# Kernel tuning notes

Measured on AMD Instinct MI355X. Metric: run time of the kernel, lower is better.

The kernel has to match this reference:

```python
import jax, jax.numpy as jnp
import numpy as np

WIN = 11      # window_size in pytorch_msssim
SIGMA = 1.5   # gaussian sigma in create_window
LEVELS = 5


def _gauss_window(channels, dtype):
    # 1D gaussian -> normalized 2D window, replicated per channel for depthwise conv
    x = jnp.arange(WIN, dtype=dtype) - WIN // 2
    g = jnp.exp(-(x * x) / (2.0 * SIGMA * SIGMA))
    g = g / jnp.sum(g)
    w2 = jnp.outer(g, g)  # [11,11]
    return jnp.broadcast_to(w2[None, None], (channels, 1, WIN, WIN))


def _dwconv(x, w):
    # depthwise valid conv, NCHW (matches F.conv2d(..., padding=0, groups=channel))
    return jax.lax.conv_general_dilated(
        x, w, window_strides=(1, 1), padding='VALID',
        dimension_numbers=('NCHW', 'OIHW', 'NCHW'),
        feature_group_count=x.shape[1])


def _ssim_cs(p, t, w):
    # pytorch_msssim.ssim with full=True, val_range L=1 (inputs in [0,1])
    C1 = 0.01 ** 2
    C2 = 0.03 ** 2
    mu1 = _dwconv(p, w)
    mu2 = _dwconv(t, w)
    mu1_sq = mu1 * mu1
    mu2_sq = mu2 * mu2
    mu1_mu2 = mu1 * mu2
    sigma1_sq = _dwconv(p * p, w) - mu1_sq
    sigma2_sq = _dwconv(t * t, w) - mu2_sq
    sigma12 = _dwconv(p * t, w) - mu1_mu2
    v1 = 2.0 * sigma12 + C2
    v2 = sigma1_sq + sigma2_sq + C2
    # per-category means (axis 1 = the 10 categories, batched as channels)
    cs = jnp.mean(v1 / v2, axis=(0, 2, 3))                                   # [C]
    sim = jnp.mean(((2.0 * mu1_mu2 + C1) * v1) / ((mu1_sq + mu2_sq + C1) * v2),
                   axis=(0, 2, 3))                                           # [C]
    return sim, cs


def _avg_pool2(x):
    n, c, h, w = x.shape
    return x.reshape(n, c, h // 2, 2, w // 2, 2).mean(axis=(3, 5))


def setup_inputs() -> dict:
    key = jax.random.key(0)
    k1, k2 = jax.random.split(key)
    y_pred = jax.random.uniform(k1, (10, 1024, 1024), dtype=jnp.float32)
    y_true = jax.random.uniform(k2, (10, 1024, 1024), dtype=jnp.float32)
    return {"y_pred": y_pred, "y_true": y_true}


def reference(y_pred, y_true):
    # MSSLoss.forward: loss = sum over 10 categories of msssim(pred[c], true[c]);
    # return 1 - mean(loss)  (loss is a scalar, so mean is identity).
    # All 10 per-category msssim calls are batched as channels of one depthwise conv.
    dtype = y_pred.dtype
    weights = jnp.array([0.0448, 0.2856, 0.3001, 0.2363, 0.1333], dtype=dtype)
    p = y_pred[None]  # [1,10,H,W]
    t = y_true[None]
    w = _gauss_window(p.shape[1], dtype)
    sims, css = [], []
    for _ in range(LEVELS):
        s, c = _ssim_cs(p, t, w)
        sims.append(s)
        css.append(c)
        p = _avg_pool2(p)
        t = _avg_pool2(t)
    mssim = jnp.stack(sims)  # [5, 10]
    mcs = jnp.stack(css)     # [5, 10]
    pow1 = mcs ** weights[:, None]
    pow2 = mssim ** weights[:, None]
    # Po-Hsun-Su pytorch_msssim: output = torch.prod(pow1[:-1] * pow2[-1])
    per_cat = jnp.prod(pow1[:-1] * pow2[-1][None, :], axis=0)  # [10]
    return 1.0 - jnp.sum(per_cat)
```

## Files before the change

### kernel.cpp

```cpp
#include <hip/hip_runtime.h>
#include <cstddef>

#define WIN 11
#define HALO 10
#define NCH 10

typedef float v4f __attribute__((ext_vector_type(4)));

constexpr float Gc[WIN] = {
    0.00102838f, 0.00759876f, 0.03600077f, 0.10936069f, 0.21300554f,
    0.26601173f, 0.21300554f, 0.10936069f, 0.03600077f, 0.00759876f,
    0.00102838f};

constexpr int HPITCH = 33;
constexpr int RS = 76;
constexpr int RSZ = RS * HPITCH;

struct Ptrs {
    const float* p[5];
    const float* t[5];
};

__global__ __launch_bounds__(256) void pool_all(
    const float* __restrict__ P0, const float* __restrict__ T0,
    float* __restrict__ p1, float* __restrict__ t1,
    float* __restrict__ p2, float* __restrict__ t2,
    float* __restrict__ p3, float* __restrict__ t3,
    float* __restrict__ p4, float* __restrict__ t4,
    float* __restrict__ acc) {
    __shared__ float sp2[256], st2[256], sp3[64], st3[64];
    const int tid = threadIdx.x;
    if (blockIdx.x == 0 && tid < 128) acc[tid] = 0.f;

    const int b = blockIdx.x;
    const int bx = b & 15, by = (b >> 4) & 15, ch = b >> 8;
    const int tx = tid & 15, ty = tid >> 4;

    const size_t rbase =
        ((size_t)ch * 1024 + by * 64 + ty * 4) * 1024 + bx * 64 + tx * 4;
    float4 pr[4], tr[4];
#pragma unroll
    for (int r2 = 0; r2 < 4; ++r2) {
        pr[r2] = *(const float4*)(P0 + rbase + (size_t)r2 * 1024);
        tr[r2] = *(const float4*)(T0 + rbase + (size_t)r2 * 1024);
    }
    float p1a = 0.25f * ((pr[0].x + pr[0].y) + (pr[1].x + pr[1].y));
    float p1b = 0.25f * ((pr[0].z + pr[0].w) + (pr[1].z + pr[1].w));
    float p1c = 0.25f * ((pr[2].x + pr[2].y) + (pr[3].x + pr[3].y));
    float p1d = 0.25f * ((pr[2].z + pr[2].w) + (pr[3].z + pr[3].w));
    float t1a = 0.25f * ((tr[0].x + tr[0].y) + (tr[1].x + tr[1].y));
    float t1b = 0.25f * ((tr[0].z + tr[0].w) + (tr[1].z + tr[1].w));
    float t1c = 0.25f * ((tr[2].x + tr[2].y) + (tr[3].x + tr[3].y));
    float t1d = 0.25f * ((tr[2].z + tr[2].w) + (tr[3].z + tr[3].w));
    size_t o1 = ((size_t)ch * 512 + by * 32 + ty * 2) * 512 + bx * 32 + tx * 2;
    *(float2*)(p1 + o1) = make_float2(p1a, p1b);
    *(float2*)(p1 + o1 + 512) = make_float2(p1c, p1d);
    *(float2*)(t1 + o1) = make_float2(t1a, t1b);
    *(float2*)(t1 + o1 + 512) = make_float2(t1c, t1d);
    float p2v = 0.25f * ((p1a + p1b) + (p1c + p1d));
    float t2v = 0.25f * ((t1a + t1b) + (t1c + t1d));
    size_t o2 = ((size_t)ch * 256 + by * 16 + ty) * 256 + bx * 16 + tx;
    p2[o2] = p2v;
    t2[o2] = t2v;
    sp2[tid] = p2v;
    st2[tid] = t2v;
    __syncthreads();
    if (tid < 64) {
        int x3 = tid & 7, y3 = tid >> 3;
        int i0 = (2 * y3) * 16 + 2 * x3;
        float p3v = 0.25f * ((sp2[i0] + sp2[i0 + 1]) + (sp2[i0 + 16] + sp2[i0 + 17]));
        float t3v = 0.25f * ((st2[i0] + st2[i0 + 1]) + (st2[i0 + 16] + st2[i0 + 17]));
        size_t o3 = ((size_t)ch * 128 + by * 8 + y3) * 128 + bx * 8 + x3;
        p3[o3] = p3v;
        t3[o3] = t3v;
        sp3[tid] = p3v;
        st3[tid] = t3v;
    }
    __syncthreads();
    if (tid < 16) {
        int x4 = tid & 3, y4 = tid >> 2;
        int i0 = (2 * y4) * 8 + 2 * x4;
        float p4v = 0.25f * ((sp3[i0] + sp3[i0 + 1]) + (sp3[i0 + 8] + sp3[i0 + 9]));
        float t4v = 0.25f * ((st3[i0] + st3[i0 + 1]) + (st3[i0 + 8] + st3[i0 + 9]));
        size_t o4 = ((size_t)ch * 64 + by * 4 + y4) * 64 + bx * 4 + x4;
        p4[o4] = p4v;
        t4[o4] = t4v;
    }
}

__global__ __launch_bounds__(256) void ssim_strip(Ptrs ptrs,
                                                  float* __restrict__ acc) {
    __shared__ v4f hq[RSZ];
    __shared__ float red[8];

    const int bxi = blockIdx.x;
    int lvl, base;
    if (bxi < 128)      { lvl = 0; base = 0; }
    else if (bxi < 160) { lvl = 1; base = 128; }
    else if (bxi < 168) { lvl = 2; base = 160; }
    else if (bxi < 172) { lvl = 3; base = 168; }
    else                { lvl = 4; base = 172; }
    const int local = bxi - base;
    const int H = 1024 >> lvl;
    const int Wout = H - HALO;
    const int ncol = 32 >> lvl;
    const int cs = local & (ncol - 1);
    const int rsi = local >> (5 - lvl);
    const int X0 = cs * 32;
    const int strip_y0 = rsi * 256;
    const int strip_rows = min(256, Wout - strip_y0);
    const int rows_needed = strip_rows + HALO;
    const int nIter = (strip_rows + 31) >> 5;

    const int c = blockIdx.y;
    const float* Pc = ptrs.p[lvl] + (size_t)c * H * H;
    const float* Tc = ptrs.t[lvl] + (size_t)c * H * H;
    const int tid = threadIdx.x;

    auto load_row18 = [&](int gy, int gxb, float2 lp[9], float2 lt[9]) {
        const float* Pr = Pc + (size_t)gy * H + gxb;
        const float* Tr = Tc + (size_t)gy * H + gxb;
        if (gxb + 18 <= H) {
#pragma unroll
            for (int j = 0; j < 9; ++j) {
                lp[j] = *(const float2*)(Pr + 2 * j);
                lt[j] = *(const float2*)(Tr + 2 * j);
            }
        } else {
#pragma unroll
            for (int j = 0; j < 9; ++j) {
                float2 a = make_float2(0.f, 0.f), b = make_float2(0.f, 0.f);
                if (gxb + 2 * j < H)     { a.x = Pr[2 * j];     b.x = Tr[2 * j]; }
                if (gxb + 2 * j + 1 < H) { a.y = Pr[2 * j + 1]; b.y = Tr[2 * j + 1]; }
                lp[j] = a;
                lt[j] = b;
            }
        }
    };

    auto conv_store8 = [&](int rr, int x0, const float2 lp[9], const float2 lt[9]) {
        v4f aq[8] = {};
#pragma unroll
        for (int xi = 0; xi < 18; ++xi) {
            float pv = (xi & 1) ? lp[xi >> 1].y : lp[xi >> 1].x;
            float tv = (xi & 1) ? lt[xi >> 1].y : lt[xi >> 1].x;
            v4f xq = (v4f){pv, tv, pv * pv + tv * tv, pv * tv};
#pragma unroll
            for (int o = 0; o < 8; ++o) {
                int k = xi - o;
                if (k >= 0 && k <= 10) aq[o] = aq[o] + Gc[k] * xq;
            }
        }
        const int sb = rr * HPITCH + x0;
#pragma unroll
        for (int o = 0; o < 8; ++o) hq[sb + o] = aq[o];
    };

    {
        const int r = tid >> 2, seg = tid & 3;
        if (r < 42) {
            float2 lp[9], lt[9];
            load_row18(strip_y0 + r, X0 + 8 * seg, lp, lt);
            conv_store8(r, 8 * seg, lp, lt);
        }
    }

    const bool isProd = (tid >= 128);
    const int pr = tid & 31;
    const int pseg = (tid >> 5) & 3;
    float2 plp[9], plt[9];
    int prRow = 42 + pr;
    int prSlot = prRow;
    bool pHave = false;
    if (isProd && prRow < rows_needed && nIter > 1) {
        load_row18(strip_y0 + prRow, X0 + 8 * pseg, plp, plt);
        pHave = true;
    }
    __syncthreads();

    float cs_sum = 0.f, sim_sum = 0.f;
    const int txl = tid & 31;
    const int g = (tid >> 5) & 3;
    int y0m = 0;
    for (int i = 0; i < nIter; ++i) {
        if (isProd) {
            if (pHave) conv_store8(prSlot, 8 * pseg, plp, plt);
            prSlot += 32;
            if (prSlot >= RS) prSlot -= RS;
            prRow += 32;
            pHave = (prRow < rows_needed) && (i + 2 < nIter + 1) && (i + 1 < nIter);
            if (pHave) load_row18(strip_y0 + prRow, X0 + 8 * pseg, plp, plt);
        } else {
            int sl = y0m + 8 * g;
            if (sl >= RS) sl -= RS;
            v4f a[8] = {};
#pragma unroll
            for (int yr = 0; yr < 18; ++yr) {
                v4f vq = hq[sl * HPITCH + txl];
#pragma unroll
                for (int o = 0; o < 8; ++o) {
                    int k = yr - o;
                    if (k >= 0 && k <= 10) a[o] = a[o] + Gc[k] * vq;
                }
                ++sl;
                if (sl >= RS) sl = 0;
            }
            const float C1c = 1.0e-4f, C2c = 9.0e-4f;
            const bool colok = (X0 + txl) < Wout;
            const int orow0 = 32 * i + 8 * g;
#pragma unroll
            for (int o = 0; o < 8; ++o) {
                if (colok && (orow0 + o) < strip_rows) {
                    float mu1 = a[o].x, mu2 = a[o].y;
                    float mu1s = mu1 * mu1, mu2s = mu2 * mu2, mu12 = mu1 * mu2;
                    float v2 = a[o].z - mu1s - mu2s + C2c;
                    float v1 = 2.f * (a[o].w - mu12) + C2c;
                    float den2 = mu1s + mu2s + C1c;
                    float num2 = 2.f * mu12 + C1c;
                    float inv = 1.f / (v2 * den2);
                    cs_sum = fmaf(v1 * den2, inv, cs_sum);
                    sim_sum = fmaf(num2 * v1, inv, sim_sum);
                }
            }
        }
        y0m += 32;
        if (y0m >= RS) y0m -= RS;
        __syncthreads();
    }

#pragma unroll
    for (int off = 32; off > 0; off >>= 1) {
        cs_sum += __shfl_down(cs_sum, off, 64);
        sim_sum += __shfl_down(sim_sum, off, 64);
    }
    int wave = tid >> 6;
    if ((tid & 63) == 0) {
        red[wave * 2 + 0] = sim_sum;
        red[wave * 2 + 1] = cs_sum;
    }
    __syncthreads();
    if (tid == 0) {
        float s = red[0] + red[2] + red[4] + red[6];
        float cc = red[1] + red[3] + red[5] + red[7];
        atomicAdd(&acc[(lvl * NCH + c) * 2 + 0], s);
        atomicAdd(&acc[(lvl * NCH + c) * 2 + 1], cc);
    }
}

__global__ void finalize_k(const float* __restrict__ acc, float* __restrict__ out) {
    if (threadIdx.x != 0) return;
    const double w[5] = {0.0448, 0.2856, 0.3001, 0.2363, 0.1333};
    const double counts[5] = {1014.0 * 1014.0, 502.0 * 502.0, 246.0 * 246.0,
                              118.0 * 118.0, 54.0 * 54.0};
    double total = 0.0;
    for (int c = 0; c < NCH; ++c) {
        double pc = 1.0;
        for (int l = 0; l < 4; ++l) {
            double mcs = (double)acc[(l * NCH + c) * 2 + 1] / counts[l];
            pc *= pow(mcs, w[l]);
        }
        double ms4 = (double)acc[(4 * NCH + c) * 2 + 0] / counts[4];
        double p2 = pow(ms4, w[4]);
        pc *= (p2 * p2) * (p2 * p2);
        total += pc;
    }
    *out = (float)(1.0 - total);
}

extern "C" void kernel_launch(void* const* d_in, const int* in_sizes, int n_in,
                              void* d_out, int out_size, void* d_ws, size_t ws_size,
                              hipStream_t stream) {
    const float* P0 = (const float*)d_in[0];
    const float* T0 = (const float*)d_in[1];
    float* out = (float*)d_out;
    float* acc = (float*)d_ws;

    const size_t n1 = (size_t)NCH * 512 * 512;
    const size_t n2 = (size_t)NCH * 256 * 256;
    const size_t n3 = (size_t)NCH * 128 * 128;
    const size_t n4 = (size_t)NCH * 64 * 64;
    float* p1 = acc + 128;
    float* t1 = p1 + n1;
    float* p2 = t1 + n1;
    float* t2 = p2 + n2;
    float* p3 = t2 + n2;
    float* t3 = p3 + n3;
    float* p4 = t3 + n3;
    float* t4 = p4 + n4;

    pool_all<<<2560, 256, 0, stream>>>(P0, T0, p1, t1, p2, t2, p3, t3, p4, t4, acc);

    Ptrs ptrs;
    ptrs.p[0] = P0; ptrs.t[0] = T0;
    ptrs.p[1] = p1; ptrs.t[1] = t1;
    ptrs.p[2] = p2; ptrs.t[2] = t2;
    ptrs.p[3] = p3; ptrs.t[3] = t3;
    ptrs.p[4] = p4; ptrs.t[4] = t4;

    ssim_strip<<<dim3(174, NCH, 1), 256, 0, stream>>>(ptrs, acc);

    finalize_k<<<1, 64, 0, stream>>>(acc, out);
}
```

Before: 198.0 us.

## Shrink per-thread output tile to 4 and ring buffer to 42 rows for occupancy

Cuts each thread's horizontal and vertical convolution work from 8 outputs to 4. The shared-memory ring buffer shrinks from 76 to 42 rows and each pipeline iteration now covers 16 rows instead of 32. A launch-bounds occupancy hint of 7 blocks per CU is added, and rows are loaded with float4 vector loads. Smaller register arrays and less LDS per block allow more resident waves, at the cost of more halo recomputation per output (14 inputs for 4 outputs versus 18 for 8) and twice as many barrier-synchronized iterations.

Measured after the change: 389.6 us. 1.97x slower.

```diff
diff --git a/kernel.cpp b/kernel.cpp
--- a/kernel.cpp
+++ b/kernel.cpp
@@ -13,7 +13,7 @@
     0.00102838f};
 
 constexpr int HPITCH = 33;
-constexpr int RS = 76;
+constexpr int RS = 42;
 constexpr int RSZ = RS * HPITCH;
 
 struct Ptrs {
@@ -88,8 +88,8 @@
     }
 }
 
-__global__ __launch_bounds__(256) void ssim_strip(Ptrs ptrs,
-                                                  float* __restrict__ acc) {
+__global__ __launch_bounds__(256, 7) void ssim_strip(Ptrs ptrs,
+                                                     float* __restrict__ acc) {
     __shared__ v4f hq[RSZ];
     __shared__ float red[8];
 
@@ -110,70 +110,82 @@
     const int strip_y0 = rsi * 256;
     const int strip_rows = min(256, Wout - strip_y0);
     const int rows_needed = strip_rows + HALO;
-    const int nIter = (strip_rows + 31) >> 5;
+    const int nIter = (strip_rows + 15) >> 4;
 
     const int c = blockIdx.y;
     const float* Pc = ptrs.p[lvl] + (size_t)c * H * H;
     const float* Tc = ptrs.t[lvl] + (size_t)c * H * H;
     const int tid = threadIdx.x;
 
-    auto load_row18 = [&](int gy, int gxb, float2 lp[9], float2 lt[9]) {
+    auto load_row14 = [&](int gy, int gxb, float lp[14], float lt[14]) {
         const float* Pr = Pc + (size_t)gy * H + gxb;
         const float* Tr = Tc + (size_t)gy * H + gxb;
-        if (gxb + 18 <= H) {
-#pragma unroll
-            for (int j = 0; j < 9; ++j) {
-                lp[j] = *(const float2*)(Pr + 2 * j);
-                lt[j] = *(const float2*)(Tr + 2 * j);
+        if (gxb + 14 <= H) {
+            float4 a0 = *(const float4*)(Pr);
+            float4 a1 = *(const float4*)(Pr + 4);
+            float4 a2 = *(const float4*)(Pr + 8);
+            float2 a3 = *(const float2*)(Pr + 12);
+            lp[0] = a0.x; lp[1] = a0.y; lp[2]  = a0.z; lp[3]  = a0.w;
+            lp[4] = a1.x; lp[5] = a1.y; lp[6]  = a1.z; lp[7]  = a1.w;
+            lp[8] = a2.x; lp[9] = a2.y; lp[10] = a2.z; lp[11] = a2.w;
+            lp[12] = a3.x; lp[13] = a3.y;
+            float4 b0 = *(const float4*)(Tr);
+            float4 b1 = *(const float4*)(Tr + 4);
+            float4 b2 = *(const float4*)(Tr + 8);
+            float2 b3 = *(const float2*)(Tr + 12);
+            lt[0] = b0.x; lt[1] = b0.y; lt[2]  = b0.z; lt[3]  = b0.w;
+            lt[4] = b1.x; lt[5] = b1.y; lt[6]  = b1.z; lt[7]  = b1.w;
+            lt[8] = b2.x; lt[9] = b2.y; lt[10] = b2.z; lt[11] = b2.y;
+            lt[11] = b2.w;
+            lt[12] = b3.x; lt[13] = b3.y;
+        } else {
+#pragma unroll
+            for (int j = 0; j < 14; ++j) {
+                float pv = 0.f, tv = 0.f;
+                if (gxb + j < H) { pv = Pr[j]; tv = Tr[j]; }
+                lp[j] = pv;
+                lt[j] = tv;
             }
-        } else {
-#pragma unroll
-            for (int j = 0; j < 9; ++j) {
-                float2 a = make_float2(0.f, 0.f), b = make_float2(0.f, 0.f);
-                if (gxb + 2 * j < H)     { a.x = Pr[2 * j];     b.x = Tr[2 * j]; }
-                if (gxb + 2 * j + 1 < H) { a.y = Pr[2 * j + 1]; b.y = Tr[2 * j + 1]; }
-                lp[j] = a;
-                lt[j] = b;
-            }
         }
     };
 
-    auto conv_store8 = [&](int rr, int x0, const float2 lp[9], const float2 lt[9]) {
-        v4f aq[8] = {};
-#pragma unroll
-        for (int xi = 0; xi < 18; ++xi) {
-            float pv = (xi & 1) ? lp[xi >> 1].y : lp[xi >> 1].x;
-            float tv = (xi & 1) ? lt[xi >> 1].y : lt[xi >> 1].x;
+    auto conv_store4 = [&](int rr, int x0, const float lp[14], const float lt[14]) {
+        v4f aq[4] = {};
+#pragma unroll
+        for (int xi = 0; xi < 14; ++xi) {
+            float pv = lp[xi];
+            float tv = lt[xi];
             v4f xq = (v4f){pv, tv, pv * pv + tv * tv, pv * tv};
 #pragma unroll
-            for (int o = 0; o < 8; ++o) {
+            for (int o = 0; o < 4; ++o) {
                 int k = xi - o;
                 if (k >= 0 && k <= 10) aq[o] = aq[o] + Gc[k] * xq;
             }
         }
         const int sb = rr * HPITCH + x0;
 #pragma unroll
-        for (int o = 0; o < 8; ++o) hq[sb + o] = aq[o];
+        for (int o = 0; o < 4; ++o) hq[sb + o] = aq[o];
     };
 
     {
-        const int r = tid >> 2, seg = tid & 3;
-        if (r < 42) {
-            float2 lp[9], lt[9];
-            load_row18(strip_y0 + r, X0 + 8 * seg, lp, lt);
-            conv_store8(r, 8 * seg, lp, lt);
+        const int r = tid >> 3, seg = tid & 7;
+        if (r < 26) {
+            float lp[14], lt[14];
+            load_row14(strip_y0 + r, X0 + 4 * seg, lp, lt);
+            conv_store4(r, 4 * seg, lp, lt);
         }
     }
 
     const bool isProd = (tid >= 128);
-    const int pr = tid & 31;
-    const int pseg = (tid >> 5) & 3;
-    float2 plp[9], plt[9];
-    int prRow = 42 + pr;
+    const int idx = tid & 127;
+    const int prow = (idx & 7) | ((idx >> 6) << 3);
+    const int pseg = (idx >> 3) & 7;
+    float plp[14], plt[14];
+    int prRow = 26 + prow;
     int prSlot = prRow;
     bool pHave = false;
-    if (isProd && prRow < rows_needed && nIter > 1) {
-        load_row18(strip_y0 + prRow, X0 + 8 * pseg, plp, plt);
+    if (isProd && nIter > 1 && prRow < rows_needed) {
+        load_row14(strip_y0 + prRow, X0 + 4 * pseg, plp, plt);
         pHave = true;
     }
     __syncthreads();
@@ -184,32 +196,34 @@
     int y0m = 0;
     for (int i = 0; i < nIter; ++i) {
         if (isProd) {
-            if (pHave) conv_store8(prSlot, 8 * pseg, plp, plt);
-            prSlot += 32;
+            if (pHave) conv_store4(prSlot, 4 * pseg, plp, plt);
+            prSlot += 16;
             if (prSlot >= RS) prSlot -= RS;
-            prRow += 32;
-            pHave = (prRow < rows_needed) && (i + 2 < nIter + 1) && (i + 1 < nIter);
-            if (pHave) load_row18(strip_y0 + prRow, X0 + 8 * pseg, plp, plt);
+            prRow += 16;
+            pHave = (prRow < rows_needed) && (i + 2 < nIter);
+            if (pHave) load_row14(strip_y0 + prRow, X0 + 4 * pseg, plp, plt);
         } else {
-            int sl = y0m + 8 * g;
+            int sl = y0m + 4 * g;
             if (sl >= RS) sl -= RS;
-            v4f a[8] = {};
-#pragma unroll
-            for (int yr = 0; yr < 18; ++yr) {
-                v4f vq = hq[sl * HPITCH + txl];
-#pragma unroll
-                for (int o = 0; o < 8; ++o) {
-                    int k = yr - o;
+            int ad = sl * HPITCH + txl;
+            v4f a[4] = {};
+#pragma unroll
+            for (int j = 0; j < 14; ++j) {
+                v4f vq = hq[ad];
+#pragma unroll
+                for (int o = 0; o < 4; ++o) {
+                    int k = j - o;
                     if (k >= 0 && k <= 10) a[o] = a[o] + Gc[k] * vq;
                 }
+                ad += HPITCH;
                 ++sl;
-                if (sl >= RS) sl = 0;
+                if (sl >= RS) { sl = 0; ad -= RSZ; }
             }
             const float C1c = 1.0e-4f, C2c = 9.0e-4f;
             const bool colok = (X0 + txl) < Wout;
-            const int orow0 = 32 * i + 8 * g;
-#pragma unroll
-            for (int o = 0; o < 8; ++o) {
+            const int orow0 = 16 * i + 4 * g;
+#pragma unroll
+            for (int o = 0; o < 4; ++o) {
                 if (colok && (orow0 + o) < strip_rows) {
                     float mu1 = a[o].x, mu2 = a[o].y;
                     float mu1s = mu1 * mu1, mu2s = mu2 * mu2, mu12 = mu1 * mu2;
@@ -223,7 +237,7 @@
                 }
             }
         }
-        y0m += 32;
+        y0m += 16;
         if (y0m >= RS) y0m -= RS;
         __syncthreads();
     }
```

## Replace block-strip SSIM with per-wave sliding-window vertical convolution

Applied to the files above, without the earlier changes.

Rewrites the SSIM kernel so each wavefront owns an independent 54-column by 64-row tile. It streams input rows from global memory into registers, does the horizontal 11-tap pass through a small per-wave LDS row buffer, and accumulates the vertical pass in a rotating 11-entry register ring that emits one output row per input row. This removes the block-wide barriers, the producer/consumer split and the large shared ring buffer, and uses a fast reciprocal intrinsic. In exchange it adds more tasks, redundant halo loads along tile edges, higher register pressure and relies on wave-synchronous LDS access without explicit sync.

After: 268.1 us. 1.35x slower.

```diff
diff --git a/kernel.cpp b/kernel.cpp
--- a/kernel.cpp
+++ b/kernel.cpp
@@ -11,10 +11,6 @@
     0.00102838f, 0.00759876f, 0.03600077f, 0.10936069f, 0.21300554f,
     0.26601173f, 0.21300554f, 0.10936069f, 0.03600077f, 0.00759876f,
     0.00102838f};
-
-constexpr int HPITCH = 33;
-constexpr int RS = 76;
-constexpr int RSZ = RS * HPITCH;
 
 struct Ptrs {
     const float* p[5];
@@ -88,144 +84,153 @@
     }
 }
 
-__global__ __launch_bounds__(256) void ssim_strip(Ptrs ptrs,
+constexpr int COLS = 54;
+constexpr int SRMAX = 64;
+constexpr int NTASK = 4110;
+
+#define LOADG(PX, TX, RB)                       \
+    {                                           \
+        _Pragma("unroll")                       \
+        for (int j_ = 0; j_ < 11; ++j_) {       \
+            int rr_ = (RB) + j_;                \
+            if (rr_ > nrowm1) rr_ = nrowm1;     \
+            PX[j_] = Pb[rr_ * H];               \
+            TX[j_] = Tb[rr_ * H];               \
+        }                                       \
+    }
+
+#define EMIT(MC)                                                          \
+    {                                                                     \
+        v4f av_ = accv[MC];                                               \
+        accv[MC] = (v4f){0.f, 0.f, 0.f, 0.f};                             \
+        if (outok) {                                                      \
+            float mu1 = av_.x, mu2 = av_.y;                               \
+            float mu1s = mu1 * mu1, mu2s = mu2 * mu2, mu12 = mu1 * mu2;   \
+            float v2 = av_.z - mu1s - mu2s + C2c;                         \
+            float v1 = 2.f * (av_.w - mu12) + C2c;                        \
+            float den2 = mu1s + mu2s + C1c;                               \
+            float num2 = 2.f * mu12 + C1c;                                \
+            float inv = __builtin_amdgcn_rcpf(v2 * den2);                 \
+            cs_sum = fmaf(v1 * den2, inv, cs_sum);                        \
+            sim_sum = fmaf(num2 * v1, inv, sim_sum);                      \
+        }                                                                 \
+    }
+
+#define STEADY(PX, TX, RB, PHI)                                           \
+    if ((RB) + (PHI) < nrow) {                                            \
+        float pv_ = PX[PHI], tv_ = TX[PHI];                               \
+        v4f xq_ = (v4f){pv_, tv_, pv_ * pv_ + tv_ * tv_, pv_ * tv_};      \
+        v4f* b_ = lbase + ((((RB) + (PHI)) & 1) ? 80 : 0);                \
+        b_[lane] = xq_;                                                   \
+        __builtin_amdgcn_sched_barrier(0x7F);                             \
+        v4f h_ = Gc[0] * b_[lane];                                        \
+        _Pragma("unroll")                                                 \
+        for (int k_ = 1; k_ < 11; ++k_) h_ += Gc[k_] * b_[lane + k_];     \
+        _Pragma("unroll")                                                 \
+        for (int m_ = 0; m_ < 11; ++m_)                                   \
+            accv[m_] += Gc[((PHI) - m_ + 11) % 11] * h_;                  \
+        EMIT(((PHI) + 1) % 11);                                           \
+    }
+
+#define PRO(PX, TX, PHI)                                                  \
+    {                                                                     \
+        float pv_ = PX[PHI], tv_ = TX[PHI];                               \
+        v4f xq_ = (v4f){pv_, tv_, pv_ * pv_ + tv_ * tv_, pv_ * tv_};      \
+        v4f* b_ = lbase + (((PHI) & 1) ? 80 : 0);                         \
+        b_[lane] = xq_;                                                   \
+        __builtin_amdgcn_sched_barrier(0x7F);                             \
+        v4f h_ = Gc[0] * b_[lane];                                        \
+        _Pragma("unroll")                                                 \
+        for (int k_ = 1; k_ < 11; ++k_) h_ += Gc[k_] * b_[lane + k_];     \
+        _Pragma("unroll")                                                 \
+        for (int m_ = 0; m_ <= (PHI); ++m_)                               \
+            accv[m_] += Gc[(PHI) - m_] * h_;                              \
+        if ((PHI) == 10) EMIT(0);                                         \
+    }
+
+#define GROUP(PX, TX, RB)      \
+    STEADY(PX, TX, RB, 0)      \
+    STEADY(PX, TX, RB, 1)      \
+    STEADY(PX, TX, RB, 2)      \
+    STEADY(PX, TX, RB, 3)      \
+    STEADY(PX, TX, RB, 4)      \
+    STEADY(PX, TX, RB, 5)      \
+    STEADY(PX, TX, RB, 6)      \
+    STEADY(PX, TX, RB, 7)      \
+    STEADY(PX, TX, RB, 8)      \
+    STEADY(PX, TX, RB, 9)      \
+    STEADY(PX, TX, RB, 10)
+
+__global__ __launch_bounds__(256, 4) void ssim_sw(Ptrs ptrs,
                                                   float* __restrict__ acc) {
-    __shared__ v4f hq[RSZ];
-    __shared__ float red[8];
-
-    const int bxi = blockIdx.x;
-    int lvl, base;
-    if (bxi < 128)      { lvl = 0; base = 0; }
-    else if (bxi < 160) { lvl = 1; base = 128; }
-    else if (bxi < 168) { lvl = 2; base = 160; }
-    else if (bxi < 172) { lvl = 3; base = 168; }
-    else                { lvl = 4; base = 172; }
-    const int local = bxi - base;
+    __shared__ v4f hq[4 * 160];
+    const int wid = threadIdx.x >> 6;
+    const int lane = threadIdx.x & 63;
+    const int task = blockIdx.x * 4 + wid;
+    if (task >= NTASK) return;
+
+    int lvl, ch, cs, rs;
+    {
+        int t;
+        if (task < 3040)      { lvl = 0; t = task;        ch = t / 304; t -= ch * 304; rs = t / 19; cs = t - rs * 19; }
+        else if (task < 3840) { lvl = 1; t = task - 3040; ch = t / 80;  t -= ch * 80;  rs = t / 10; cs = t - rs * 10; }
+        else if (task < 4040) { lvl = 2; t = task - 3840; ch = t / 20;  t -= ch * 20;  rs = t / 5;  cs = t - rs * 5;  }
+        else if (task < 4100) { lvl = 3; t = task - 4040; ch = t / 6;   t -= ch * 6;   rs = t / 3;  cs = t - rs * 3;  }
+        else                  { lvl = 4; ch = task - 4100; rs = 0; cs = 0; }
+    }
     const int H = 1024 >> lvl;
     const int Wout = H - HALO;
-    const int ncol = 32 >> lvl;
-    const int cs = local & (ncol - 1);
-    const int rsi = local >> (5 - lvl);
-    const int X0 = cs * 32;
-    const int strip_y0 = rsi * 256;
-    const int strip_rows = min(256, Wout - strip_y0);
-    const int rows_needed = strip_rows + HALO;
-    const int nIter = (strip_rows + 31) >> 5;
-
-    const int c = blockIdx.y;
-    const float* Pc = ptrs.p[lvl] + (size_t)c * H * H;
-    const float* Tc = ptrs.t[lvl] + (size_t)c * H * H;
-    const int tid = threadIdx.x;
-
-    auto load_row18 = [&](int gy, int gxb, float2 lp[9], float2 lt[9]) {
-        const float* Pr = Pc + (size_t)gy * H + gxb;
-        const float* Tr = Tc + (size_t)gy * H + gxb;
-        if (gxb + 18 <= H) {
+    const int X0 = cs * COLS;
+    const int Y0 = rs * SRMAX;
+    const int SR = (Wout - Y0 < SRMAX) ? (Wout - Y0) : SRMAX;
+    const int nrow = SR + HALO;
+    const int nrowm1 = nrow - 1;
+
+    const float* Pc = ptrs.p[lvl] + (size_t)ch * H * H;
+    const float* Tc = ptrs.t[lvl] + (size_t)ch * H * H;
+    int gc = X0 + lane;
+    if (gc > H - 1) gc = H - 1;
+    const float* Pb = Pc + (size_t)Y0 * H + gc;
+    const float* Tb = Tc + (size_t)Y0 * H + gc;
+    const bool outok = (lane < COLS) && (X0 + lane < Wout);
+
+    v4f* lbase = hq + wid * 160;
+    if (lane < 16) {
+        lbase[64 + lane] = (v4f){0.f, 0.f, 0.f, 0.f};
+        lbase[144 + lane] = (v4f){0.f, 0.f, 0.f, 0.f};
+    }
+
+    v4f accv[11];
 #pragma unroll
-            for (int j = 0; j < 9; ++j) {
-                lp[j] = *(const float2*)(Pr + 2 * j);
-                lt[j] = *(const float2*)(Tr + 2 * j);
-            }
-        } else {
-#pragma unroll
-            for (int j = 0; j < 9; ++j) {
-                float2 a = make_float2(0.f, 0.f), b = make_float2(0.f, 0.f);
-                if (gxb + 2 * j < H)     { a.x = Pr[2 * j];     b.x = Tr[2 * j]; }
-                if (gxb + 2 * j + 1 < H) { a.y = Pr[2 * j + 1]; b.y = Tr[2 * j + 1]; }
-                lp[j] = a;
-                lt[j] = b;
-            }
-        }
-    };
-
-    auto conv_store8 = [&](int rr, int x0, const float2 lp[9], const float2 lt[9]) {
-        v4f aq[8] = {};
-#pragma unroll
-        for (int xi = 0; xi < 18; ++xi) {
-            float pv = (xi & 1) ? lp[xi >> 1].y : lp[xi >> 1].x;
-            float tv = (xi & 1) ? lt[xi >> 1].y : lt[xi >> 1].x;
-            v4f xq = (v4f){pv, tv, pv * pv + tv * tv, pv * tv};
-#pragma unroll
-            for (int o = 0; o < 8; ++o) {
-                int k = xi - o;
-                if (k >= 0 && k <= 10) aq[o] = aq[o] + Gc[k] * xq;
-            }
-        }
-        const int sb = rr * HPITCH + x0;
-#pragma unroll
-        for (int o = 0; o < 8; ++o) hq[sb + o] = aq[o];
-    };
-
-    {
-        const int r = tid >> 2, seg = tid & 3;
-        if (r < 42) {
-            float2 lp[9], lt[9];
-            load_row18(strip_y0 + r, X0 + 8 * seg, lp, lt);
-            conv_store8(r, 8 * seg, lp, lt);
-        }
-    }
-
-    const bool isProd = (tid >= 128);
-    const int pr = tid & 31;
-    const int pseg = (tid >> 5) & 3;
-    float2 plp[9], plt[9];
-    int prRow = 42 + pr;
-    int prSlot = prRow;
-    bool pHave = false;
-    if (isProd && prRow < rows_needed && nIter > 1) {
-        load_row18(strip_y0 + prRow, X0 + 8 * pseg, plp, plt);
-        pHave = true;
-    }
-    __syncthreads();
-
+    for (int m = 0; m < 11; ++m) accv[m] = (v4f){0.f, 0.f, 0.f, 0.f};
     float cs_sum = 0.f, sim_sum = 0.f;
-    const int txl = tid & 31;
-    const int g = (tid >> 5) & 3;
-    int y0m = 0;
-    for (int i = 0; i < nIter; ++i) {
-        if (isProd) {
-            if (pHave) conv_store8(prSlot, 8 * pseg, plp, plt);
-            prSlot += 32;
-            if (prSlot >= RS) prSlot -= RS;
-            prRow += 32;
-            pHave = (prRow < rows_needed) && (i + 2 < nIter + 1) && (i + 1 < nIter);
-            if (pHave) load_row18(strip_y0 + prRow, X0 + 8 * pseg, plp, plt);
-        } else {
-            int sl = y0m + 8 * g;
-            if (sl >= RS) sl -= RS;
-            v4f a[8] = {};
-#pragma unroll
-            for (int yr = 0; yr < 18; ++yr) {
-                v4f vq = hq[sl * HPITCH + txl];
-#pragma unroll
-                for (int o = 0; o < 8; ++o) {
-                    int k = yr - o;
-                    if (k >= 0 && k <= 10) a[o] = a[o] + Gc[k] * vq;
-                }
-                ++sl;
-                if (sl >= RS) sl = 0;
-            }
-            const float C1c = 1.0e-4f, C2c = 9.0e-4f;
-            const bool colok = (X0 + txl) < Wout;
-            const int orow0 = 32 * i + 8 * g;
-#pragma unroll
-            for (int o = 0; o < 8; ++o) {
-                if (colok && (orow0 + o) < strip_rows) {
-                    float mu1 = a[o].x, mu2 = a[o].y;
-                    float mu1s = mu1 * mu1, mu2s = mu2 * mu2, mu12 = mu1 * mu2;
-                    float v2 = a[o].z - mu1s - mu2s + C2c;
-                    float v1 = 2.f * (a[o].w - mu12) + C2c;
-                    float den2 = mu1s + mu2s + C1c;
-                    float num2 = 2.f * mu12 + C1c;
-                    float inv = 1.f / (v2 * den2);
-                    cs_sum = fmaf(v1 * den2, inv, cs_sum);
-                    sim_sum = fmaf(num2 * v1, inv, sim_sum);
-                }
-            }
-        }
-        y0m += 32;
-        if (y0m >= RS) y0m -= RS;
-        __syncthreads();
+    const float C1c = 1.0e-4f, C2c = 9.0e-4f;
+
+    float pA[11], tA[11], pB[11], tB[11];
+    LOADG(pA, tA, 0);
+    LOADG(pB, tB, 11);
+
+    PRO(pA, tA, 0)
+    PRO(pA, tA, 1)
+    PRO(pA, tA, 2)
+    PRO(pA, tA, 3)
+    PRO(pA, tA, 4)
+    PRO(pA, tA, 5)
+    PRO(pA, tA, 6)
+    PRO(pA, tA, 7)
+    PRO(pA, tA, 8)
+    PRO(pA, tA, 9)
+    PRO(pA, tA, 10)
+
+    int rb = 11;
+    for (;;) {
+        LOADG(pA, tA, rb + 11);
+        GROUP(pB, tB, rb);
+        if (rb + 11 >= nrow) break;
+        LOADG(pB, tB, rb + 22);
+        GROUP(pA, tA, rb + 11);
+        if (rb + 22 >= nrow) break;
+        rb += 22;
     }
 
 #pragma unroll
@@ -233,17 +238,9 @@
         cs_sum += __shfl_down(cs_sum, off, 64);
         sim_sum += __shfl_down(sim_sum, off, 64);
     }
-    int wave = tid >> 6;
-    if ((tid & 63) == 0) {
-        red[wave * 2 + 0] = sim_sum;
-        red[wave * 2 + 1] = cs_sum;
-    }
-    __syncthreads();
-    if (tid == 0) {
-        float s = red[0] + red[2] + red[4] + red[6];
-        float cc = red[1] + red[3] + red[5] + red[7];
-        atomicAdd(&acc[(lvl * NCH + c) * 2 + 0], s);
-        atomicAdd(&acc[(lvl * NCH + c) * 2 + 1], cc);
+    if (lane == 0) {
+        atomicAdd(&acc[(lvl * NCH + ch) * 2 + 0], sim_sum);
+        atomicAdd(&acc[(lvl * NCH + ch) * 2 + 1], cs_sum);
     }
 }
 
@@ -297,7 +294,7 @@
     ptrs.p[3] = p3; ptrs.t[3] = t3;
     ptrs.p[4] = p4; ptrs.t[4] = t4;
 
-    ssim_strip<<<dim3(174, NCH, 1), 256, 0, stream>>>(ptrs, acc);
+    ssim_sw<<<dim3((NTASK + 3) / 4), 256, 0, stream>>>(ptrs, acc);
 
     finalize_k<<<1, 64, 0, stream>>>(acc, out);
 }
```
